# Performance work log

Measured on AMD Instinct MI355X. Metric: run time of the kernel, lower is better.

Reference implementation:

```python
import jax, jax.numpy as jnp
import numpy as np

N_NODES = 50000
N_EDGES = 800000
F_IN = 256
HID = 64
HEADS = 4
N_CLASSES = 2
N_GRAPHS = 512


def setup_inputs() -> dict:
    key = jax.random.key(0)
    ks = jax.random.split(key, 20)
    s = 0.05
    x = jax.random.normal(ks[0], (N_NODES, F_IN), jnp.float32)
    edge_index = jax.random.randint(ks[1], (2, N_EDGES), 0, N_NODES, jnp.int32)
    batch = jnp.sort(jax.random.randint(ks[2], (N_NODES,), 0, N_GRAPHS, jnp.int32))
    return {
        "x": x, "edge_index": edge_index, "batch": batch,
        # conv1: GATConv(F_IN, HID, heads=HEADS, concat=True)
        "W1": jax.random.normal(ks[3], (F_IN, HEADS * HID), jnp.float32) * s,
        "att_src1": jax.random.normal(ks[4], (HEADS, HID), jnp.float32) * s,
        "att_dst1": jax.random.normal(ks[5], (HEADS, HID), jnp.float32) * s,
        "b1": jnp.zeros((HEADS * HID,), jnp.float32),
        # conv2: GATConv(HEADS*HID, HID, heads=1, concat=False)
        "W2": jax.random.normal(ks[6], (HEADS * HID, HID), jnp.float32) * s,
        "att_src2": jax.random.normal(ks[7], (1, HID), jnp.float32) * s,
        "att_dst2": jax.random.normal(ks[8], (1, HID), jnp.float32) * s,
        "b2": jnp.zeros((HID,), jnp.float32),
        # global attention linear
        "Wg": jax.random.normal(ks[9], (HID, 1), jnp.float32) * s,
        "bg": jnp.zeros((1,), jnp.float32),
        # classifier
        "Wc1": jax.random.normal(ks[10], (HID, HID // 2), jnp.float32) * s,
        "bc1": jnp.zeros((HID // 2,), jnp.float32),
        "Wc2": jax.random.normal(ks[11], (HID // 2, N_CLASSES), jnp.float32) * s,
        "bc2": jnp.zeros((N_CLASSES,), jnp.float32),
    }


def _add_self_loops(edge_index, num_nodes):
    ar = jnp.arange(num_nodes, dtype=edge_index.dtype)
    return jnp.concatenate([edge_index, jnp.stack([ar, ar])], axis=1)


def _gat_conv(x, edge_index, W, a_src, a_dst, b, concat):
    # PyG GATConv (eval mode): h = xW, e = leaky_relu(a_s.h_src + a_d.h_dst),
    # alpha = segment_softmax(e, dst), out = scatter_add(alpha * h_src, dst)
    N = x.shape[0]
    H, C = a_src.shape
    h = (x @ W).reshape(N, H, C)                      # [N,H,C]
    src, dst = edge_index[0], edge_index[1]
    asrc = jnp.sum(h * a_src[None], axis=-1)          # [N,H]
    adst = jnp.sum(h * a_dst[None], axis=-1)          # [N,H]
    e = jax.nn.leaky_relu(asrc[src] + adst[dst], 0.2) # [E,H]
    emax = jax.ops.segment_max(e, dst, num_segments=N)
    e = jnp.exp(e - emax[dst])
    denom = jax.ops.segment_sum(e, dst, num_segments=N)
    alpha = e / (denom[dst] + 1e-16)                  # [E,H]
    msg = alpha[:, :, None] * h[src]                  # [E,H,C]
    out = jax.ops.segment_sum(msg, dst, num_segments=N)  # [N,H,C]
    out = out.reshape(N, H * C) if concat else out.mean(axis=1)
    return out + b


def _segment_softmax(v, seg, num_segments):
    m = jax.ops.segment_max(v, seg, num_segments=num_segments)
    e = jnp.exp(v - m[seg])
    s = jax.ops.segment_sum(e, seg, num_segments=num_segments)
    return e / (s[seg] + 1e-16)


def reference(x, edge_index, batch, W1, att_src1, att_dst1, b1,
              W2, att_src2, att_dst2, b2, Wg, bg, Wc1, bc1, Wc2, bc2):
    N = x.shape[0]
    ei = _add_self_loops(edge_index, N)
    h = _gat_conv(x, ei, W1, att_src1, att_dst1, b1, concat=True)
    h = jax.nn.elu(h)
    h = _gat_conv(h, ei, W2, att_src2, att_dst2, b2, concat=False)
    h = jax.nn.elu(h)                                  # [N,HID]
    att = (h @ Wg + bg)[:, 0]                          # [N]
    att = _segment_softmax(att, batch, N_GRAPHS)       # softmax over nodes per graph
    h = h * att[:, None]
    pooled = jax.ops.segment_sum(h, batch, num_segments=N_GRAPHS)  # [G,HID]
    hid = jax.nn.relu(pooled @ Wc1 + bc1)
    return hid @ Wc2 + bc2                             # [G, num_classes]
```

## Files before the change

### kernel.cpp

```cpp
#include <hip/hip_runtime.h>
#include <hip/hip_bf16.h>
#include <hip/hip_fp16.h>
#include <math.h>

#define N_NODES 50000
#define N_EDGES 800000
#define M_EDGES (N_EDGES + N_NODES)
#define NGRAPH 512
#define CH1 128
#define CH2 64

typedef __attribute__((ext_vector_type(8))) short bfrag8;
typedef __attribute__((ext_vector_type(4))) float floatx4;

__device__ __forceinline__ float wave_max(float v){
  #pragma unroll
  for (int o = 32; o; o >>= 1) v = fmaxf(v, __shfl_xor(v, o));
  return v;
}
__device__ __forceinline__ float wave_sum(float v){
  #pragma unroll
  for (int o = 32; o; o >>= 1) v += __shfl_xor(v, o);
  return v;
}
__device__ __forceinline__ unsigned short f2bf(float f){
  union { float f; unsigned int u; } v; v.f = f;
  unsigned int r = v.u + 0x7FFFu + ((v.u >> 16) & 1u);
  return (unsigned short)(r >> 16);
}
__device__ __forceinline__ float bf2f(unsigned short h){
  union { unsigned int u; float f; } v; v.u = ((unsigned int)h) << 16; return v.f;
}

__global__ void k_count(const int* __restrict__ ei, int* __restrict__ deg){
  int e = blockIdx.x * blockDim.x + threadIdx.x;
  if (e >= M_EDGES) return;
  int dst = (e < N_EDGES) ? ei[N_EDGES + e] : (e - N_EDGES);
  atomicAdd(&deg[dst], 1);
}
__global__ void k_alloc(const int* __restrict__ deg, int* __restrict__ row_start,
                        int* __restrict__ cursor){
  int n = blockIdx.x * blockDim.x + threadIdx.x;
  if (n >= N_NODES) return;
  row_start[n] = atomicAdd(cursor, deg[n]);
}
__global__ void k_fill(const int* __restrict__ ei, const int* __restrict__ row_start,
                       int* __restrict__ fill, int* __restrict__ col){
  int e = blockIdx.x * blockDim.x + threadIdx.x;
  if (e >= M_EDGES) return;
  int src, dst;
  if (e < N_EDGES){ src = ei[e]; dst = ei[N_EDGES + e]; }
  else { src = dst = e - N_EDGES; }
  int slot = row_start[dst] + atomicAdd(&fill[dst], 1);
  col[slot] = src;
}

__global__ __launch_bounds__(256) void k_projP(const float* __restrict__ W1,
                                               const float* __restrict__ as1,
                                               const float* __restrict__ ad1,
                                               float* __restrict__ P){
  int k = threadIdx.x;
  float acc[8] = {0.f,0.f,0.f,0.f,0.f,0.f,0.f,0.f};
  for (int c = 0; c < 64; ++c){
    #pragma unroll
    for (int h = 0; h < 4; ++h){
      float w = W1[k * 256 + h * 64 + c];
      acc[h]     += w * as1[h * 64 + c];
      acc[4 + h] += w * ad1[h * 64 + c];
    }
  }
  #pragma unroll
  for (int j = 0; j < 8; ++j) P[k * 8 + j] = acc[j];
}

__global__ __launch_bounds__(256) void k_att1p(const float* __restrict__ x,
                                               const float* __restrict__ P,
                                               float* __restrict__ asrc,
                                               float* __restrict__ adst,
                                               unsigned short* __restrict__ x2){
  __shared__ float Ps[256][9];
  const int tid = threadIdx.x;
  #pragma unroll
  for (int j = 0; j < 8; ++j) Ps[tid][j] = P[tid * 8 + j];
  __syncthreads();
  const int n = blockIdx.x * 4 + (tid >> 6);
  const int lane = tid & 63;
  float4 xv = *(const float4*)&x[(size_t)n * 256 + lane * 4];
  ushort4 hi4, lo4;
  hi4.x = f2bf(xv.x); lo4.x = f2bf(xv.x - bf2f(hi4.x));
  hi4.y = f2bf(xv.y); lo4.y = f2bf(xv.y - bf2f(hi4.y));
  hi4.z = f2bf(xv.z); lo4.z = f2bf(xv.z - bf2f(hi4.z));
  hi4.w = f2bf(xv.w); lo4.w = f2bf(xv.w - bf2f(hi4.w));
  *(ushort4*)&x2[(size_t)n * 512 + lane * 4] = hi4;
  *(ushort4*)&x2[(size_t)n * 512 + 256 + lane * 4] = lo4;
  float p[8];
  #pragma unroll
  for (int j = 0; j < 8; ++j){
    p[j] = xv.x * Ps[lane * 4 + 0][j] + xv.y * Ps[lane * 4 + 1][j]
         + xv.z * Ps[lane * 4 + 2][j] + xv.w * Ps[lane * 4 + 3][j];
    p[j] = wave_sum(p[j]);
  }
  if (lane == 0){
    *(float4*)&asrc[n * 4] = make_float4(p[0], p[1], p[2], p[3]);
    *(float4*)&adst[n * 4] = make_float4(p[4], p[5], p[6], p[7]);
  }
}

__global__ void k_splitW(const float* __restrict__ W, unsigned short* __restrict__ Bt,
                         int Ncols){
  int n = blockIdx.x, k = threadIdx.x;
  float w = W[(size_t)(k & 255) * Ncols + n];
  unsigned short hi = f2bf(w);
  Bt[(size_t)n * 768 + k] = (k < 512) ? hi : f2bf(w - bf2f(hi));
}

template<int OUT_HALF>
__global__ __launch_bounds__(256) void mfma_gemm(const unsigned short* __restrict__ A,
                                                 const unsigned short* __restrict__ Bt,
                                                 void* __restrict__ Cout,
                                                 int M, int ldc){
  __shared__ unsigned short As[128 * 64];
  __shared__ unsigned short Bs[64 * 64];
  const int tid = threadIdx.x;
  const int m0 = blockIdx.y * 128, n0 = blockIdx.x * 64;
  floatx4 acc[4][2];
  #pragma unroll
  for (int mr = 0; mr < 4; ++mr)
    #pragma unroll
    for (int nr = 0; nr < 2; ++nr) acc[mr][nr] = (floatx4){0.f, 0.f, 0.f, 0.f};
  const int l = tid & 63, w = tid >> 6;
  const int wm = (w >> 1) * 64, wn = (w & 1) * 32;
  const int lr = l & 15;

  for (int kc = 0; kc < 768; kc += 64){
    #pragma unroll
    for (int i = 0; i < 4; ++i){
      int f = tid + i * 256, row = f >> 3, seg = f & 7;
      int sseg = seg ^ (row & 7);
      float4 v = make_float4(0.f, 0.f, 0.f, 0.f);
      if (m0 + row < M)
        v = *(const float4*)&A[(size_t)(m0 + row) * 512 + (kc & 511) + seg * 8];
      *(float4*)&As[row * 64 + sseg * 8] = v;
    }
    #pragma unroll
    for (int i = 0; i < 2; ++i){
      int f = tid + i * 256, row = f >> 3, seg = f & 7;
      int sseg = seg ^ (row & 7);
      *(float4*)&Bs[row * 64 + sseg * 8] =
        *(const float4*)&Bt[(size_t)(n0 + row) * 768 + kc + seg * 8];
    }
    __syncthreads();
    #pragma unroll
    for (int kk = 0; kk < 2; ++kk){
      const int seg = kk * 4 + (l >> 4);
      const int br0 = wn + lr, br1 = wn + 16 + lr;
      bfrag8 b0  = *(const bfrag8*)&Bs[br0 * 64 + (seg ^ (br0 & 7)) * 8];
      bfrag8 b1v = *(const bfrag8*)&Bs[br1 * 64 + (seg ^ (br1 & 7)) * 8];
      #pragma unroll
      for (int mr = 0; mr < 4; ++mr){
        const int ar = wm + mr * 16 + lr;
        bfrag8 a = *(const bfrag8*)&As[ar * 64 + (seg ^ (ar & 7)) * 8];
        acc[mr][0] = __builtin_amdgcn_mfma_f32_16x16x32_bf16(a, b0, acc[mr][0], 0, 0, 0);
        acc[mr][1] = __builtin_amdgcn_mfma_f32_16x16x32_bf16(a, b1v, acc[mr][1], 0, 0, 0);
      }
    }
    __syncthreads();
  }
  #pragma unroll
  for (int mr = 0; mr < 4; ++mr)
    #pragma unroll
    for (int nr = 0; nr < 2; ++nr){
      const int colg = n0 + wn + nr * 16 + lr;
      #pragma unroll
      for (int r = 0; r < 4; ++r){
        const int row = m0 + wm + mr * 16 + (l >> 4) * 4 + r;
        if (row < M){
          if (OUT_HALF)
            ((__half*)Cout)[(size_t)row * ldc + colg] = __float2half(acc[mr][nr][r]);
          else
            ((float*)Cout)[(size_t)row * ldc + colg] = acc[mr][nr][r];
        }
      }
    }
}

__global__ __launch_bounds__(256) void k_agg1(const __half* __restrict__ h1,
                                              const int* __restrict__ col,
                                              const int* __restrict__ row_start,
                                              const int* __restrict__ degv,
                                              const float* __restrict__ asrc,
                                              const float* __restrict__ adst,
                                              const float* __restrict__ b1,
                                              unsigned short* __restrict__ out1s){
  __shared__ int    src_s[CH1];
  __shared__ float4 w4_s[CH1];
  __shared__ float  redm[4][4];
  __shared__ float  reds[4][4];
  __shared__ float  mh4[4], sh4[4];
  __shared__ float4 racc[4][64];
  const int n = blockIdx.x, tid = threadIdx.x;
  const int wv = tid >> 6, lane = tid & 63;
  const int base = row_start[n], dg = degv[n];
  const float4 ad4 = *(const float4*)&adst[(size_t)n * 4];

  float lm0 = -3e38f, lm1 = -3e38f, lm2 = -3e38f, lm3 = -3e38f;
  for (int j = tid; j < dg; j += 256){
    const float4 s4 = *(const float4*)&asrc[(size_t)col[base + j] * 4];
    float e0 = s4.x + ad4.x; e0 = e0 > 0.f ? e0 : 0.2f * e0; lm0 = fmaxf(lm0, e0);
    float e1 = s4.y + ad4.y; e1 = e1 > 0.f ? e1 : 0.2f * e1; lm1 = fmaxf(lm1, e1);
    float e2 = s4.z + ad4.z; e2 = e2 > 0.f ? e2 : 0.2f * e2; lm2 = fmaxf(lm2, e2);
    float e3 = s4.w + ad4.w; e3 = e3 > 0.f ? e3 : 0.2f * e3; lm3 = fmaxf(lm3, e3);
  }
  lm0 = wave_max(lm0); lm1 = wave_max(lm1); lm2 = wave_max(lm2); lm3 = wave_max(lm3);
  if (lane == 0){ redm[wv][0] = lm0; redm[wv][1] = lm1; redm[wv][2] = lm2; redm[wv][3] = lm3; }
  __syncthreads();
  if (tid < 4)
    mh4[tid] = fmaxf(fmaxf(redm[0][tid], redm[1][tid]), fmaxf(redm[2][tid], redm[3][tid]));
  __syncthreads();
  const float m0 = mh4[0], m1 = mh4[1], m2 = mh4[2], m3 = mh4[3];

  float ls0 = 0.f, ls1 = 0.f, ls2 = 0.f, ls3 = 0.f;
  float4 acc = make_float4(0.f, 0.f, 0.f, 0.f);
  const int hsel = lane >> 4;
  for (int c0 = 0; c0 < dg; c0 += CH1){
    const int cnt = min(CH1, dg - c0);
    __syncthreads();
    if (tid < cnt){
      const int src = col[base + c0 + tid];
      const float4 s4 = *(const float4*)&asrc[(size_t)src * 4];
      float e0 = s4.x + ad4.x; e0 = e0 > 0.f ? e0 : 0.2f * e0; float w0 = __expf(e0 - m0);
      float e1 = s4.y + ad4.y; e1 = e1 > 0.f ? e1 : 0.2f * e1; float w1 = __expf(e1 - m1);
      float e2 = s4.z + ad4.z; e2 = e2 > 0.f ? e2 : 0.2f * e2; float w2 = __expf(e2 - m2);
      float e3 = s4.w + ad4.w; e3 = e3 > 0.f ? e3 : 0.2f * e3; float w3 = __expf(e3 - m3);
      ls0 += w0; ls1 += w1; ls2 += w2; ls3 += w3;
      src_s[tid] = src;
      w4_s[tid] = make_float4(w0, w1, w2, w3);
    }
    __syncthreads();
    int j = wv;
    for (; j + 12 < cnt; j += 16){
      float wt[4]; uint2 rw[4];
      #pragma unroll
      for (int u = 0; u < 4; ++u){
        wt[u] = ((const float*)&w4_s[j + u * 4])[hsel];
        rw[u] = *(const uint2*)&h1[(size_t)src_s[j + u * 4] * 256 + lane * 4];
      }
      #pragma unroll
      for (int u = 0; u < 4; ++u){
        float2 f01 = __half22float2(*reinterpret_cast<const __half2*>(&rw[u].x));
        float2 f23 = __half22float2(*reinterpret_cast<const __half2*>(&rw[u].y));
        acc.x += wt[u] * f01.x; acc.y += wt[u] * f01.y;
        acc.z += wt[u] * f23.x; acc.w += wt[u] * f23.y;
      }
    }
    for (; j < cnt; j += 4){
      const float wt = ((const float*)&w4_s[j])[hsel];
      const uint2 rw = *(const uint2*)&h1[(size_t)src_s[j] * 256 + lane * 4];
      float2 f01 = __half22float2(*reinterpret_cast<const __half2*>(&rw.x));
      float2 f23 = __half22float2(*reinterpret_cast<const __half2*>(&rw.y));
      acc.x += wt * f01.x; acc.y += wt * f01.y;
      acc.z += wt * f23.x; acc.w += wt * f23.y;
    }
  }
  ls0 = wave_sum(ls0); ls1 = wave_sum(ls1); ls2 = wave_sum(ls2); ls3 = wave_sum(ls3);
  if (lane == 0){ reds[wv][0] = ls0; reds[wv][1] = ls1; reds[wv][2] = ls2; reds[wv][3] = ls3; }
  racc[wv][lane] = acc;
  __syncthreads();
  if (tid < 4) sh4[tid] = reds[0][tid] + reds[1][tid] + reds[2][tid] + reds[3][tid];
  __syncthreads();
  const float inv = 1.f / (sh4[tid >> 6] + 1e-16f);
  const int c4 = tid >> 2, cm = tid & 3;
  float v = ((const float*)&racc[0][c4])[cm] + ((const float*)&racc[1][c4])[cm]
          + ((const float*)&racc[2][c4])[cm] + ((const float*)&racc[3][c4])[cm];
  float o = v * inv + b1[tid];
  o = o > 0.f ? o : __expf(o) - 1.f;
  unsigned short hi = f2bf(o);
  out1s[(size_t)n * 512 + tid] = hi;
  out1s[(size_t)n * 512 + 256 + tid] = f2bf(o - bf2f(hi));
}

__global__ __launch_bounds__(64) void k_att2(const __half* __restrict__ t2,
                                             const float* __restrict__ a_src,
                                             const float* __restrict__ a_dst,
                                             float* __restrict__ asrc,
                                             float* __restrict__ adst){
  int n = blockIdx.x, lane = threadIdx.x;
  float v = __half2float(t2[(size_t)n * 64 + lane]);
  float ps = wave_sum(v * a_src[lane]);
  float pd = wave_sum(v * a_dst[lane]);
  if (lane == 0){ asrc[n] = ps; adst[n] = pd; }
}

__global__ __launch_bounds__(64) void k_agg2(const __half* __restrict__ t2,
                                             const int* __restrict__ col,
                                             const int* __restrict__ row_start,
                                             const int* __restrict__ degv,
                                             const float* __restrict__ asrc,
                                             const float* __restrict__ adst,
                                             const float* __restrict__ b2,
                                             const float* __restrict__ Wg,
                                             const float* __restrict__ bg,
                                             float* __restrict__ hf,
                                             float* __restrict__ attg){
  __shared__ int   src_s[CH2];
  __shared__ float w_s[CH2];
  const int n = blockIdx.x, lane = threadIdx.x;
  const int base = row_start[n], dg = degv[n];
  const float ad = adst[n];
  float lm = -3e38f;
  for (int j = lane; j < dg; j += 64){
    float e = asrc[col[base + j]] + ad;
    e = e > 0.f ? e : 0.2f * e;
    lm = fmaxf(lm, e);
  }
  lm = wave_max(lm);
  float ls = 0.f;
  float4 acc = make_float4(0.f, 0.f, 0.f, 0.f);
  const int eg = lane >> 4, c4 = (lane & 15) * 4;
  for (int c0 = 0; c0 < dg; c0 += CH2){
    const int cnt = min(CH2, dg - c0);
    __syncthreads();
    if (lane < cnt){
      const int src = col[base + c0 + lane];
      float e = asrc[src] + ad;
      e = e > 0.f ? e : 0.2f * e;
      float w = __expf(e - lm);
      ls += w;
      src_s[lane] = src;
      w_s[lane] = w;
    }
    __syncthreads();
    for (int j = eg; j < cnt; j += 4){
      const float wt = w_s[j];
      const uint2 rw = *(const uint2*)&t2[(size_t)src_s[j] * 64 + c4];
      float2 f01 = __half22float2(*reinterpret_cast<const __half2*>(&rw.x));
      float2 f23 = __half22float2(*reinterpret_cast<const __half2*>(&rw.y));
      acc.x += wt * f01.x; acc.y += wt * f01.y;
      acc.z += wt * f23.x; acc.w += wt * f23.y;
    }
  }
  ls = wave_sum(ls);
  #pragma unroll
  for (int o = 16; o <= 32; o <<= 1){
    acc.x += __shfl_xor(acc.x, o); acc.y += __shfl_xor(acc.y, o);
    acc.z += __shfl_xor(acc.z, o); acc.w += __shfl_xor(acc.w, o);
  }
  const float inv = 1.f / (ls + 1e-16f);
  float o0 = acc.x * inv + b2[c4 + 0]; o0 = o0 > 0.f ? o0 : __expf(o0) - 1.f;
  float o1 = acc.y * inv + b2[c4 + 1]; o1 = o1 > 0.f ? o1 : __expf(o1) - 1.f;
  float o2 = acc.z * inv + b2[c4 + 2]; o2 = o2 > 0.f ? o2 : __expf(o2) - 1.f;
  float o3 = acc.w * inv + b2[c4 + 3]; o3 = o3 > 0.f ? o3 : __expf(o3) - 1.f;
  if (eg == 0) *(float4*)&hf[(size_t)n * 64 + c4] = make_float4(o0, o1, o2, o3);
  float p = (eg == 0)
          ? (o0 * Wg[c4] + o1 * Wg[c4 + 1] + o2 * Wg[c4 + 2] + o3 * Wg[c4 + 3]) : 0.f;
  p = wave_sum(p);
  if (lane == 0) attg[n] = p + bg[0];
}

__global__ __launch_bounds__(64) void k_pool(const float* __restrict__ hf,
                                             const float* __restrict__ attg,
                                             const int* __restrict__ batch,
                                             const float* __restrict__ Wc1,
                                             const float* __restrict__ bc1,
                                             const float* __restrict__ Wc2,
                                             const float* __restrict__ bc2,
                                             float* __restrict__ out){
  __shared__ float pooled[64];
  __shared__ float hid[32];
  const int g = blockIdx.x, lane = threadIdx.x;
  int lo = 0, hi = N_NODES;
  while (lo < hi){ int mid = (lo + hi) >> 1; if (batch[mid] < g) lo = mid + 1; else hi = mid; }
  const int s0 = lo;
  hi = N_NODES;
  while (lo < hi){ int mid = (lo + hi) >> 1; if (batch[mid] < g + 1) lo = mid + 1; else hi = mid; }
  const int s1 = lo;
  float lm = -3e38f;
  for (int j = s0 + lane; j < s1; j += 64) lm = fmaxf(lm, attg[j]);
  lm = wave_max(lm);
  float ls = 0.f;
  for (int j = s0 + lane; j < s1; j += 64) ls += __expf(attg[j] - lm);
  ls = wave_sum(ls);
  const float inv = 1.f / (ls + 1e-16f);
  float acc = 0.f;
  for (int j = s0; j < s1; ++j)
    acc += __expf(attg[j] - lm) * hf[(size_t)j * 64 + lane];
  pooled[lane] = acc * inv;
  __syncthreads();
  if (lane < 32){
    float t = bc1[lane];
    #pragma unroll
    for (int c = 0; c < 64; ++c) t += pooled[c] * Wc1[c * 32 + lane];
    hid[lane] = t > 0.f ? t : 0.f;
  }
  __syncthreads();
  if (lane < 2){
    float t = bc2[lane];
    #pragma unroll
    for (int c = 0; c < 32; ++c) t += hid[c] * Wc2[c * 2 + lane];
    out[g * 2 + lane] = t;
  }
}

extern "C" void kernel_launch(void* const* d_in, const int* in_sizes, int n_in,
                              void* d_out, int out_size, void* d_ws, size_t ws_size,
                              hipStream_t stream){
  const float* x    = (const float*)d_in[0];
  const int*   ei   = (const int*)d_in[1];
  const int*   batch= (const int*)d_in[2];
  const float* W1   = (const float*)d_in[3];
  const float* as1  = (const float*)d_in[4];
  const float* ad1  = (const float*)d_in[5];
  const float* b1   = (const float*)d_in[6];
  const float* W2   = (const float*)d_in[7];
  const float* as2  = (const float*)d_in[8];
  const float* ad2  = (const float*)d_in[9];
  const float* b2   = (const float*)d_in[10];
  const float* Wg   = (const float*)d_in[11];
  const float* bg   = (const float*)d_in[12];
  const float* Wc1  = (const float*)d_in[13];
  const float* bc1  = (const float*)d_in[14];
  const float* Wc2  = (const float*)d_in[15];
  const float* bc2  = (const float*)d_in[16];

  char* ws = (char*)d_ws;
  unsigned short* x2s   = (unsigned short*)(ws + 0LL);
  unsigned short* out1s = (unsigned short*)(ws + 0LL);
  __half* h1h   = (__half*)(ws + 51200000LL);
  __half* t2h   = (__half*)(ws + 102400000LL);
  float* hf     = (float*)(ws + 115200000LL);
  float* P      = (float*)(ws + 115200000LL);
  unsigned short* W1B3t = (unsigned short*)(ws + 115208192LL);
  unsigned short* W2B3t = (unsigned short*)(ws + 115601408LL);
  float* asrc1  = (float*)(ws + 128000000LL);
  float* adst1  = (float*)(ws + 128800000LL);
  float* asrc2  = (float*)(ws + 129600000LL);
  float* adst2  = (float*)(ws + 129800000LL);
  float* attg   = (float*)(ws + 130000000LL);
  int*   deg    = (int*)  (ws + 130200000LL);
  int*   fill   = (int*)  (ws + 130400000LL);
  int*   cursor = (int*)  (ws + 130600000LL);
  int*   row_st = (int*)  (ws + 130600256LL);
  int*   col    = (int*)  (ws + 130800256LL);
  float* outf   = (float*)d_out;

  hipMemsetAsync(ws + 130200000LL, 0, 400256, stream);

  k_count<<<(M_EDGES + 255) / 256, 256, 0, stream>>>(ei, deg);
  k_alloc<<<(N_NODES + 255) / 256, 256, 0, stream>>>(deg, row_st, cursor);
  k_fill<<<(M_EDGES + 255) / 256, 256, 0, stream>>>(ei, row_st, fill, col);

  k_projP<<<1, 256, 0, stream>>>(W1, as1, ad1, P);
  k_att1p<<<N_NODES / 4, 256, 0, stream>>>(x, P, asrc1, adst1, x2s);
  k_splitW<<<256, 768, 0, stream>>>(W1, W1B3t, 256);
  k_splitW<<<64, 768, 0, stream>>>(W2, W2B3t, 64);

  mfma_gemm<1><<<dim3(4, 391), 256, 0, stream>>>(x2s, W1B3t, (void*)h1h, N_NODES, 256);
  k_agg1<<<N_NODES, 256, 0, stream>>>(h1h, col, row_st, deg, asrc1, adst1, b1, out1s);

  mfma_gemm<1><<<dim3(1, 391), 256, 0, stream>>>(out1s, W2B3t, (void*)t2h, N_NODES, 64);
  k_att2<<<N_NODES, 64, 0, stream>>>(t2h, as2, ad2, asrc2, adst2);
  k_agg2<<<N_NODES, 64, 0, stream>>>(t2h, col, row_st, deg, asrc2, adst2, b2, Wg, bg, hf, attg);

  k_pool<<<NGRAPH, 64, 0, stream>>>(hf, attg, batch, Wc1, bc1, Wc2, bc2, outf);
}
```

Before: 555.8 us.

## Process one node per wavefront with online softmax in GAT aggregation kernels

The GAT aggregation kernels move from one block per node to one wavefront per node, four nodes per block. Edge weights and source indices are shared through wave shuffles instead of LDS and barriers, and a single-pass online softmax replaces the separate max pass. The three weight-preparation kernels are merged into one launch, and k_att2 now packs four nodes per block. The aim is to cut per-node block overhead, barriers and the extra edge pass, at the cost of less parallelism per high-degree node and more shuffle instructions.

```diff
diff --git a/kernel.cpp b/kernel.cpp
--- a/kernel.cpp
+++ b/kernel.cpp
@@ -7,8 +7,6 @@
 #define N_EDGES 800000
 #define M_EDGES (N_EDGES + N_NODES)
 #define NGRAPH 512
-#define CH1 128
-#define CH2 64
 
 typedef __attribute__((ext_vector_type(8))) short bfrag8;
 typedef __attribute__((ext_vector_type(4))) float floatx4;
@@ -55,22 +53,36 @@
   col[slot] = src;
 }
 
-__global__ __launch_bounds__(256) void k_projP(const float* __restrict__ W1,
-                                               const float* __restrict__ as1,
-                                               const float* __restrict__ ad1,
-                                               float* __restrict__ P){
-  int k = threadIdx.x;
-  float acc[8] = {0.f,0.f,0.f,0.f,0.f,0.f,0.f,0.f};
-  for (int c = 0; c < 64; ++c){
-    #pragma unroll
-    for (int h = 0; h < 4; ++h){
-      float w = W1[k * 256 + h * 64 + c];
-      acc[h]     += w * as1[h * 64 + c];
-      acc[4 + h] += w * ad1[h * 64 + c];
-    }
-  }
-  #pragma unroll
-  for (int j = 0; j < 8; ++j) P[k * 8 + j] = acc[j];
+__global__ __launch_bounds__(768) void k_prep(const float* __restrict__ W1,
+                                              const float* __restrict__ W2,
+                                              const float* __restrict__ as1,
+                                              const float* __restrict__ ad1,
+                                              unsigned short* __restrict__ W1B3t,
+                                              unsigned short* __restrict__ W2B3t,
+                                              float* __restrict__ P){
+  const int b = blockIdx.x, k = threadIdx.x;
+  if (b < 256){
+    float w = W1[(size_t)(k & 255) * 256 + b];
+    unsigned short hi = f2bf(w);
+    W1B3t[(size_t)b * 768 + k] = (k < 512) ? hi : f2bf(w - bf2f(hi));
+  } else if (b < 320){
+    int n = b - 256;
+    float w = W2[(size_t)(k & 255) * 64 + n];
+    unsigned short hi = f2bf(w);
+    W2B3t[(size_t)n * 768 + k] = (k < 512) ? hi : f2bf(w - bf2f(hi));
+  } else if (k < 256){
+    float acc[8] = {0.f,0.f,0.f,0.f,0.f,0.f,0.f,0.f};
+    for (int c = 0; c < 64; ++c){
+      #pragma unroll
+      for (int h = 0; h < 4; ++h){
+        float w = W1[k * 256 + h * 64 + c];
+        acc[h]     += w * as1[h * 64 + c];
+        acc[4 + h] += w * ad1[h * 64 + c];
+      }
+    }
+    #pragma unroll
+    for (int j = 0; j < 8; ++j) P[k * 8 + j] = acc[j];
+  }
 }
 
 __global__ __launch_bounds__(256) void k_att1p(const float* __restrict__ x,
@@ -106,14 +118,6 @@
   }
 }
 
-__global__ void k_splitW(const float* __restrict__ W, unsigned short* __restrict__ Bt,
-                         int Ncols){
-  int n = blockIdx.x, k = threadIdx.x;
-  float w = W[(size_t)(k & 255) * Ncols + n];
-  unsigned short hi = f2bf(w);
-  Bt[(size_t)n * 768 + k] = (k < 512) ? hi : f2bf(w - bf2f(hi));
-}
-
 template<int OUT_HALF>
 __global__ __launch_bounds__(256) void mfma_gemm(const unsigned short* __restrict__ A,
                                                  const unsigned short* __restrict__ Bt,
@@ -184,67 +188,62 @@
     }
 }
 
-__global__ __launch_bounds__(256) void k_agg1(const __half* __restrict__ h1,
-                                              const int* __restrict__ col,
-                                              const int* __restrict__ row_start,
-                                              const int* __restrict__ degv,
-                                              const float* __restrict__ asrc,
-                                              const float* __restrict__ adst,
-                                              const float* __restrict__ b1,
-                                              unsigned short* __restrict__ out1s){
-  __shared__ int    src_s[CH1];
-  __shared__ float4 w4_s[CH1];
-  __shared__ float  redm[4][4];
-  __shared__ float  reds[4][4];
-  __shared__ float  mh4[4], sh4[4];
-  __shared__ float4 racc[4][64];
-  const int n = blockIdx.x, tid = threadIdx.x;
-  const int wv = tid >> 6, lane = tid & 63;
+__global__ __launch_bounds__(256) void k_agg1w(const __half* __restrict__ h1,
+                                               const int* __restrict__ col,
+                                               const int* __restrict__ row_start,
+                                               const int* __restrict__ degv,
+                                               const float* __restrict__ asrc,
+                                               const float* __restrict__ adst,
+                                               const float* __restrict__ b1,
+                                               unsigned short* __restrict__ out1s){
+  const int tid = threadIdx.x, wv = tid >> 6, lane = tid & 63;
+  const int n = blockIdx.x * 4 + wv;
   const int base = row_start[n], dg = degv[n];
   const float4 ad4 = *(const float4*)&adst[(size_t)n * 4];
-
-  float lm0 = -3e38f, lm1 = -3e38f, lm2 = -3e38f, lm3 = -3e38f;
-  for (int j = tid; j < dg; j += 256){
-    const float4 s4 = *(const float4*)&asrc[(size_t)col[base + j] * 4];
-    float e0 = s4.x + ad4.x; e0 = e0 > 0.f ? e0 : 0.2f * e0; lm0 = fmaxf(lm0, e0);
-    float e1 = s4.y + ad4.y; e1 = e1 > 0.f ? e1 : 0.2f * e1; lm1 = fmaxf(lm1, e1);
-    float e2 = s4.z + ad4.z; e2 = e2 > 0.f ? e2 : 0.2f * e2; lm2 = fmaxf(lm2, e2);
-    float e3 = s4.w + ad4.w; e3 = e3 > 0.f ? e3 : 0.2f * e3; lm3 = fmaxf(lm3, e3);
-  }
-  lm0 = wave_max(lm0); lm1 = wave_max(lm1); lm2 = wave_max(lm2); lm3 = wave_max(lm3);
-  if (lane == 0){ redm[wv][0] = lm0; redm[wv][1] = lm1; redm[wv][2] = lm2; redm[wv][3] = lm3; }
-  __syncthreads();
-  if (tid < 4)
-    mh4[tid] = fmaxf(fmaxf(redm[0][tid], redm[1][tid]), fmaxf(redm[2][tid], redm[3][tid]));
-  __syncthreads();
-  const float m0 = mh4[0], m1 = mh4[1], m2 = mh4[2], m3 = mh4[3];
-
-  float ls0 = 0.f, ls1 = 0.f, ls2 = 0.f, ls3 = 0.f;
+  const int hsel = lane >> 4;
+  float m0 = -3e38f, m1 = -3e38f, m2 = -3e38f, m3 = -3e38f;
+  float s = 0.f;
   float4 acc = make_float4(0.f, 0.f, 0.f, 0.f);
-  const int hsel = lane >> 4;
-  for (int c0 = 0; c0 < dg; c0 += CH1){
-    const int cnt = min(CH1, dg - c0);
-    __syncthreads();
-    if (tid < cnt){
-      const int src = col[base + c0 + tid];
+
+  for (int c0 = 0; c0 < dg; c0 += 64){
+    const int cnt = min(64, dg - c0);
+    float e0 = -3e38f, e1 = -3e38f, e2 = -3e38f, e3 = -3e38f;
+    int src = 0;
+    if (lane < cnt){
+      src = col[base + c0 + lane];
       const float4 s4 = *(const float4*)&asrc[(size_t)src * 4];
-      float e0 = s4.x + ad4.x; e0 = e0 > 0.f ? e0 : 0.2f * e0; float w0 = __expf(e0 - m0);
-      float e1 = s4.y + ad4.y; e1 = e1 > 0.f ? e1 : 0.2f * e1; float w1 = __expf(e1 - m1);
-      float e2 = s4.z + ad4.z; e2 = e2 > 0.f ? e2 : 0.2f * e2; float w2 = __expf(e2 - m2);
-      float e3 = s4.w + ad4.w; e3 = e3 > 0.f ? e3 : 0.2f * e3; float w3 = __expf(e3 - m3);
-      ls0 += w0; ls1 += w1; ls2 += w2; ls3 += w3;
-      src_s[tid] = src;
-      w4_s[tid] = make_float4(w0, w1, w2, w3);
-    }
-    __syncthreads();
-    int j = wv;
-    for (; j + 12 < cnt; j += 16){
-      float wt[4]; uint2 rw[4];
+      e0 = s4.x + ad4.x; e0 = e0 > 0.f ? e0 : 0.2f * e0;
+      e1 = s4.y + ad4.y; e1 = e1 > 0.f ? e1 : 0.2f * e1;
+      e2 = s4.z + ad4.z; e2 = e2 > 0.f ? e2 : 0.2f * e2;
+      e3 = s4.w + ad4.w; e3 = e3 > 0.f ? e3 : 0.2f * e3;
+    }
+    const float M0 = wave_max(e0), M1 = wave_max(e1), M2 = wave_max(e2), M3 = wave_max(e3);
+    const float nm0 = fmaxf(m0, M0), nm1 = fmaxf(m1, M1);
+    const float nm2 = fmaxf(m2, M2), nm3 = fmaxf(m3, M3);
+    const float mo = hsel == 0 ? m0 : hsel == 1 ? m1 : hsel == 2 ? m2 : m3;
+    const float mn = hsel == 0 ? nm0 : hsel == 1 ? nm1 : hsel == 2 ? nm2 : nm3;
+    const float r = __expf(mo - mn);
+    s *= r; acc.x *= r; acc.y *= r; acc.z *= r; acc.w *= r;
+    m0 = nm0; m1 = nm1; m2 = nm2; m3 = nm3;
+    const float w0 = __expf(e0 - nm0), w1 = __expf(e1 - nm1);
+    const float w2 = __expf(e2 - nm2), w3 = __expf(e3 - nm3);
+    const float S0 = wave_sum(w0), S1 = wave_sum(w1);
+    const float S2 = wave_sum(w2), S3 = wave_sum(w3);
+    s += hsel == 0 ? S0 : hsel == 1 ? S1 : hsel == 2 ? S2 : S3;
+    int j = 0;
+    for (; j + 4 <= cnt; j += 4){
+      float wt[4]; int sj[4];
       #pragma unroll
       for (int u = 0; u < 4; ++u){
-        wt[u] = ((const float*)&w4_s[j + u * 4])[hsel];
-        rw[u] = *(const uint2*)&h1[(size_t)src_s[j + u * 4] * 256 + lane * 4];
-      }
+        const float t0 = __shfl(w0, j + u), t1 = __shfl(w1, j + u);
+        const float t2 = __shfl(w2, j + u), t3 = __shfl(w3, j + u);
+        wt[u] = hsel == 0 ? t0 : hsel == 1 ? t1 : hsel == 2 ? t2 : t3;
+        sj[u] = __shfl(src, j + u);
+      }
+      uint2 rw[4];
+      #pragma unroll
+      for (int u = 0; u < 4; ++u)
+        rw[u] = *(const uint2*)&h1[(size_t)sj[u] * 256 + lane * 4];
       #pragma unroll
       for (int u = 0; u < 4; ++u){
         float2 f01 = __half22float2(*reinterpret_cast<const __half2*>(&rw[u].x));
@@ -253,106 +252,101 @@
         acc.z += wt[u] * f23.x; acc.w += wt[u] * f23.y;
       }
     }
-    for (; j < cnt; j += 4){
-      const float wt = ((const float*)&w4_s[j])[hsel];
-      const uint2 rw = *(const uint2*)&h1[(size_t)src_s[j] * 256 + lane * 4];
+    for (; j < cnt; ++j){
+      const float t0 = __shfl(w0, j), t1 = __shfl(w1, j);
+      const float t2 = __shfl(w2, j), t3 = __shfl(w3, j);
+      const float wt = hsel == 0 ? t0 : hsel == 1 ? t1 : hsel == 2 ? t2 : t3;
+      const int sj = __shfl(src, j);
+      const uint2 rw = *(const uint2*)&h1[(size_t)sj * 256 + lane * 4];
       float2 f01 = __half22float2(*reinterpret_cast<const __half2*>(&rw.x));
       float2 f23 = __half22float2(*reinterpret_cast<const __half2*>(&rw.y));
       acc.x += wt * f01.x; acc.y += wt * f01.y;
       acc.z += wt * f23.x; acc.w += wt * f23.y;
     }
   }
-  ls0 = wave_sum(ls0); ls1 = wave_sum(ls1); ls2 = wave_sum(ls2); ls3 = wave_sum(ls3);
-  if (lane == 0){ reds[wv][0] = ls0; reds[wv][1] = ls1; reds[wv][2] = ls2; reds[wv][3] = ls3; }
-  racc[wv][lane] = acc;
-  __syncthreads();
-  if (tid < 4) sh4[tid] = reds[0][tid] + reds[1][tid] + reds[2][tid] + reds[3][tid];
-  __syncthreads();
-  const float inv = 1.f / (sh4[tid >> 6] + 1e-16f);
-  const int c4 = tid >> 2, cm = tid & 3;
-  float v = ((const float*)&racc[0][c4])[cm] + ((const float*)&racc[1][c4])[cm]
-          + ((const float*)&racc[2][c4])[cm] + ((const float*)&racc[3][c4])[cm];
-  float o = v * inv + b1[tid];
-  o = o > 0.f ? o : __expf(o) - 1.f;
-  unsigned short hi = f2bf(o);
-  out1s[(size_t)n * 512 + tid] = hi;
-  out1s[(size_t)n * 512 + 256 + tid] = f2bf(o - bf2f(hi));
-}
-
-__global__ __launch_bounds__(64) void k_att2(const __half* __restrict__ t2,
-                                             const float* __restrict__ a_src,
-                                             const float* __restrict__ a_dst,
-                                             float* __restrict__ asrc,
-                                             float* __restrict__ adst){
-  int n = blockIdx.x, lane = threadIdx.x;
+  const float inv = 1.f / (s + 1e-16f);
+  const float4 bb = *(const float4*)&b1[lane * 4];
+  float o0 = acc.x * inv + bb.x; o0 = o0 > 0.f ? o0 : __expf(o0) - 1.f;
+  float o1 = acc.y * inv + bb.y; o1 = o1 > 0.f ? o1 : __expf(o1) - 1.f;
+  float o2 = acc.z * inv + bb.z; o2 = o2 > 0.f ? o2 : __expf(o2) - 1.f;
+  float o3 = acc.w * inv + bb.w; o3 = o3 > 0.f ? o3 : __expf(o3) - 1.f;
+  ushort4 hi4, lo4;
+  hi4.x = f2bf(o0); lo4.x = f2bf(o0 - bf2f(hi4.x));
+  hi4.y = f2bf(o1); lo4.y = f2bf(o1 - bf2f(hi4.y));
+  hi4.z = f2bf(o2); lo4.z = f2bf(o2 - bf2f(hi4.z));
+  hi4.w = f2bf(o3); lo4.w = f2bf(o3 - bf2f(hi4.w));
+  *(ushort4*)&out1s[(size_t)n * 512 + lane * 4] = hi4;
+  *(ushort4*)&out1s[(size_t)n * 512 + 256 + lane * 4] = lo4;
+}
+
+__global__ __launch_bounds__(256) void k_att2(const __half* __restrict__ t2,
+                                              const float* __restrict__ a_src,
+                                              const float* __restrict__ a_dst,
+                                              float* __restrict__ asrc,
+                                              float* __restrict__ adst){
+  const int tid = threadIdx.x, wv = tid >> 6, lane = tid & 63;
+  const int n = blockIdx.x * 4 + wv;
   float v = __half2float(t2[(size_t)n * 64 + lane]);
   float ps = wave_sum(v * a_src[lane]);
   float pd = wave_sum(v * a_dst[lane]);
   if (lane == 0){ asrc[n] = ps; adst[n] = pd; }
 }
 
-__global__ __launch_bounds__(64) void k_agg2(const __half* __restrict__ t2,
-                                             const int* __restrict__ col,
-                                             const int* __restrict__ row_start,
-                                             const int* __restrict__ degv,
-                                             const float* __restrict__ asrc,
-                                             const float* __restrict__ adst,
-                                             const float* __restrict__ b2,
-                                             const float* __restrict__ Wg,
-                                             const float* __restrict__ bg,
-                                             float* __restrict__ hf,
-                                             float* __restrict__ attg){
-  __shared__ int   src_s[CH2];
-  __shared__ float w_s[CH2];
-  const int n = blockIdx.x, lane = threadIdx.x;
+__global__ __launch_bounds__(256) void k_agg2w(const __half* __restrict__ t2,
+                                               const int* __restrict__ col,
+                                               const int* __restrict__ row_start,
+                                               const int* __restrict__ degv,
+                                               const float* __restrict__ asrc,
+                                               const float* __restrict__ adst,
+                                               const float* __restrict__ b2,
+                                               const float* __restrict__ Wg,
+                                               const float* __restrict__ bg,
+                                               float* __restrict__ hf,
+                                               float* __restrict__ attg){
+  const int tid = threadIdx.x, wv = tid >> 6, lane = tid & 63;
+  const int n = blockIdx.x * 4 + wv;
   const int base = row_start[n], dg = degv[n];
   const float ad = adst[n];
-  float lm = -3e38f;
-  for (int j = lane; j < dg; j += 64){
-    float e = asrc[col[base + j]] + ad;
-    e = e > 0.f ? e : 0.2f * e;
-    lm = fmaxf(lm, e);
-  }
-  lm = wave_max(lm);
-  float ls = 0.f;
-  float4 acc = make_float4(0.f, 0.f, 0.f, 0.f);
-  const int eg = lane >> 4, c4 = (lane & 15) * 4;
-  for (int c0 = 0; c0 < dg; c0 += CH2){
-    const int cnt = min(CH2, dg - c0);
-    __syncthreads();
+  const int half = lane >> 5, c2 = lane & 31;
+  float m = -3e38f, s = 0.f;
+  float2 acc = make_float2(0.f, 0.f);
+
+  for (int c0 = 0; c0 < dg; c0 += 64){
+    const int cnt = min(64, dg - c0);
+    float e = -3e38f; int src = 0;
     if (lane < cnt){
-      const int src = col[base + c0 + lane];
-      float e = asrc[src] + ad;
+      src = col[base + c0 + lane];
+      e = asrc[src] + ad;
       e = e > 0.f ? e : 0.2f * e;
-      float w = __expf(e - lm);
-      ls += w;
-      src_s[lane] = src;
-      w_s[lane] = w;
-    }
-    __syncthreads();
-    for (int j = eg; j < cnt; j += 4){
-      const float wt = w_s[j];
-      const uint2 rw = *(const uint2*)&t2[(size_t)src_s[j] * 64 + c4];
-      float2 f01 = __half22float2(*reinterpret_cast<const __half2*>(&rw.x));
-      float2 f23 = __half22float2(*reinterpret_cast<const __half2*>(&rw.y));
-      acc.x += wt * f01.x; acc.y += wt * f01.y;
-      acc.z += wt * f23.x; acc.w += wt * f23.y;
-    }
-  }
-  ls = wave_sum(ls);
-  #pragma unroll
-  for (int o = 16; o <= 32; o <<= 1){
-    acc.x += __shfl_xor(acc.x, o); acc.y += __shfl_xor(acc.y, o);
-    acc.z += __shfl_xor(acc.z, o); acc.w += __shfl_xor(acc.w, o);
-  }
-  const float inv = 1.f / (ls + 1e-16f);
-  float o0 = acc.x * inv + b2[c4 + 0]; o0 = o0 > 0.f ? o0 : __expf(o0) - 1.f;
-  float o1 = acc.y * inv + b2[c4 + 1]; o1 = o1 > 0.f ? o1 : __expf(o1) - 1.f;
-  float o2 = acc.z * inv + b2[c4 + 2]; o2 = o2 > 0.f ? o2 : __expf(o2) - 1.f;
-  float o3 = acc.w * inv + b2[c4 + 3]; o3 = o3 > 0.f ? o3 : __expf(o3) - 1.f;
-  if (eg == 0) *(float4*)&hf[(size_t)n * 64 + c4] = make_float4(o0, o1, o2, o3);
-  float p = (eg == 0)
-          ? (o0 * Wg[c4] + o1 * Wg[c4 + 1] + o2 * Wg[c4 + 2] + o3 * Wg[c4 + 3]) : 0.f;
+    }
+    const float M = wave_max(e);
+    const float mn = fmaxf(m, M);
+    const float r = __expf(m - mn);
+    s *= r; acc.x *= r; acc.y *= r;
+    m = mn;
+    const float w = __expf(e - mn);
+    s += wave_sum(w);
+    for (int j = 0; j < cnt; j += 2){
+      const int j0 = j + half;
+      if (j0 < cnt){
+        const float wt = __shfl(w, j0);
+        const int sj = __shfl(src, j0);
+        const unsigned int rw = *(const unsigned int*)&t2[(size_t)sj * 64 + c2 * 2];
+        float2 f = __half22float2(*reinterpret_cast<const __half2*>(&rw));
+        acc.x += wt * f.x; acc.y += wt * f.y;
+      }
+    }
+  }
+  acc.x += __shfl_xor(acc.x, 32);
+  acc.y += __shfl_xor(acc.y, 32);
+  const float inv = 1.f / (s + 1e-16f);
+  float p = 0.f;
+  if (half == 0){
+    float o0 = acc.x * inv + b2[c2 * 2];     o0 = o0 > 0.f ? o0 : __expf(o0) - 1.f;
+    float o1 = acc.y * inv + b2[c2 * 2 + 1]; o1 = o1 > 0.f ? o1 : __expf(o1) - 1.f;
+    *(float2*)&hf[(size_t)n * 64 + c2 * 2] = make_float2(o0, o1);
+    p = o0 * Wg[c2 * 2] + o1 * Wg[c2 * 2 + 1];
+  }
   p = wave_sum(p);
   if (lane == 0) attg[n] = p + bg[0];
 }
@@ -449,17 +443,15 @@
   k_alloc<<<(N_NODES + 255) / 256, 256, 0, stream>>>(deg, row_st, cursor);
   k_fill<<<(M_EDGES + 255) / 256, 256, 0, stream>>>(ei, row_st, fill, col);
 
-  k_projP<<<1, 256, 0, stream>>>(W1, as1, ad1, P);
+  k_prep<<<321, 768, 0, stream>>>(W1, W2, as1, ad1, W1B3t, W2B3t, P);
   k_att1p<<<N_NODES / 4, 256, 0, stream>>>(x, P, asrc1, adst1, x2s);
-  k_splitW<<<256, 768, 0, stream>>>(W1, W1B3t, 256);
-  k_splitW<<<64, 768, 0, stream>>>(W2, W2B3t, 64);
 
   mfma_gemm<1><<<dim3(4, 391), 256, 0, stream>>>(x2s, W1B3t, (void*)h1h, N_NODES, 256);
-  k_agg1<<<N_NODES, 256, 0, stream>>>(h1h, col, row_st, deg, asrc1, adst1, b1, out1s);
+  k_agg1w<<<N_NODES / 4, 256, 0, stream>>>(h1h, col, row_st, deg, asrc1, adst1, b1, out1s);
 
   mfma_gemm<1><<<dim3(1, 391), 256, 0, stream>>>(out1s, W2B3t, (void*)t2h, N_NODES, 64);
-  k_att2<<<N_NODES, 64, 0, stream>>>(t2h, as2, ad2, asrc2, adst2);
-  k_agg2<<<N_NODES, 64, 0, stream>>>(t2h, col, row_st, deg, asrc2, adst2, b2, Wg, bg, hf, attg);
+  k_att2<<<N_NODES / 4, 256, 0, stream>>>(t2h, as2, ad2, asrc2, adst2);
+  k_agg2w<<<N_NODES / 4, 256, 0, stream>>>(t2h, col, row_st, deg, asrc2, adst2, b2, Wg, bg, hf, attg);
 
   k_pool<<<NGRAPH, 64, 0, stream>>>(hf, attg, batch, Wc1, bc1, Wc2, bc2, outf);
 }
```

New measurement: 508.9 us. 1.09x faster.
